# Kernel tuning notes

Measured on AMD Instinct MI355X. Metric: run time of the kernel, lower is better.

Reference implementation:

```python
import jax, jax.numpy as jnp
import numpy as np

N = 40000      # nodes
E = 20000      # hyperedges
M = 640000     # incidences
D = 128        # num_features == num_classes == MLP_hidden
ALPHA = 0.1
EPS = 1e-5


def _layernorm(h, g, b):
    mu = jnp.mean(h, axis=-1, keepdims=True)
    var = jnp.mean((h - mu) ** 2, axis=-1, keepdims=True)
    return (h - mu) * jax.lax.rsqrt(var + EPS) * g + b


def _mlp(x, w1, b1, g, be, w2, b2):
    h = x @ w1 + b1
    h = jax.nn.relu(_layernorm(h, g, be))
    return h @ w2 + b2


def _scatter_mean(vals, idx, num_segments):
    s = jax.ops.segment_sum(vals, idx, num_segments=num_segments)
    cnt = jax.ops.segment_sum(jnp.ones((vals.shape[0],), vals.dtype), idx,
                              num_segments=num_segments)
    return s / jnp.maximum(cnt, 1.0)[:, None]


def setup_inputs() -> dict:
    key = jax.random.key(0)
    ks = jax.random.split(key, 16)
    x = jax.random.normal(ks[0], (N, D), dtype=jnp.float32)
    vertex = jax.random.randint(ks[1], (M,), 0, N)
    edges = jax.random.randint(ks[2], (M,), 0, E)
    edge_index = jnp.stack([vertex, edges]).astype(jnp.int64)

    def lin(k, fin, fout):
        s = 1.0 / np.sqrt(fin)
        kw, kb = jax.random.split(k)
        return (jax.random.uniform(kw, (fin, fout), jnp.float32, -s, s),
                jax.random.uniform(kb, (fout,), jnp.float32, -s, s))

    w1_1, b1_1 = lin(ks[3], D, D)
    w1_2, b1_2 = lin(ks[4], D, D)
    w2_1, b2_1 = lin(ks[5], 2 * D, D)
    w2_2, b2_2 = lin(ks[6], D, D)
    g1 = jnp.ones((D,), jnp.float32)
    be1 = jnp.zeros((D,), jnp.float32)
    g2 = jnp.ones((D,), jnp.float32)
    be2 = jnp.zeros((D,), jnp.float32)
    return {"x": x, "w1_1": w1_1, "b1_1": b1_1, "g1": g1, "be1": be1,
            "w1_2": w1_2, "b1_2": b1_2, "w2_1": w2_1, "b2_1": b2_1,
            "g2": g2, "be2": be2, "w2_2": w2_2, "b2_2": b2_2,
            "edge_index": edge_index}


def reference(x, w1_1, b1_1, g1, be1, w1_2, b1_2,
              w2_1, b2_1, g2, be2, w2_2, b2_2, edge_index):
    vertex = edge_index[0]
    edges = edge_index[1]
    X0 = x
    # gather -> MLP1 -> scatter-mean onto hyperedges
    Xve = _mlp(x[vertex], w1_1, b1_1, g1, be1, w1_2, b1_2)   # [M, D]
    Xe = _scatter_mean(Xve, edges, E)                         # [E, D]
    # gather back -> concat -> MLP2 -> scatter-mean onto nodes
    Xev = Xe[edges]                                           # [M, D]
    Xev = _mlp(jnp.concatenate([x[vertex], Xev], axis=-1),
               w2_1, b2_1, g2, be2, w2_2, b2_2)               # [M, D]
    Xv = _scatter_mean(Xev, vertex, N)                        # [N, D]
    return (1.0 - ALPHA) * Xv + ALPHA * X0
```

## Files before the change

### kernel.cpp

```cpp
#include <hip/hip_runtime.h>

#define DF 128
constexpr int NN = 40000;
constexpr int EE = 20000;
constexpr int MM = 640000;
constexpr float EPSF = 1e-5f;
constexpr float ALPHA = 0.1f;
constexpr int SE = 96;
constexpr int SV = 64;

constexpr int NB_G1 = (NN + 63) / 64;
constexpr int NB_G2 = (NN + 63) / 64;
constexpr int NB_CB = (128 * 128 + 128 + 255) / 256;
constexpr int NB_GEMMS = NB_G1 + NB_G2 + NB_CB;
constexpr int NB_BUILD = 5000;

__device__ __forceinline__ int cidxE(int e) { return (e & 7) * (EE >> 3) + (e >> 3); }
__device__ __forceinline__ int cidxV(int v) { return (v & 7) * (NN >> 3) + (v >> 3); }

template <int EPI, bool STATS>
__device__ __forceinline__ void gemm_tile(const float* __restrict__ A, int nrows,
                                          const float* __restrict__ W,
                                          const float* __restrict__ bias,
                                          const float* __restrict__ bias2,
                                          const int* __restrict__ cnt,
                                          const float* __restrict__ g,
                                          const float* __restrict__ be,
                                          const float* __restrict__ xres,
                                          float* __restrict__ C,
                                          float* __restrict__ sOut,
                                          float* __restrict__ qOut,
                                          int blk, float* as) {
  int tid = threadIdx.x;
  int rbase = blk * 64;

  #pragma unroll
  for (int j = 0; j < 8; ++j) {
    int q = tid + j * 256;
    int row = q >> 5;
    int c4 = q & 31;
    int grow = rbase + row;
    float4 v = make_float4(0.f, 0.f, 0.f, 0.f);
    if (grow < nrows) {
      v = *reinterpret_cast<const float4*>(A + (size_t)grow * DF + c4 * 4);
    }
    *reinterpret_cast<float4*>(&as[row * 132 + c4 * 4]) = v;
  }
  __syncthreads();

  int tc = tid & 15;
  int tr = tid >> 4;
  int cbase = tc * 8;

  float acc[4][8];
  #pragma unroll
  for (int i = 0; i < 4; ++i)
    #pragma unroll
    for (int c = 0; c < 8; ++c) acc[i][c] = 0.0f;

  #pragma unroll 4
  for (int k = 0; k < 128; ++k) {
    float w[8];
    *reinterpret_cast<float4*>(&w[0]) = *reinterpret_cast<const float4*>(W + k * DF + cbase);
    *reinterpret_cast<float4*>(&w[4]) = *reinterpret_cast<const float4*>(W + k * DF + cbase + 4);
    float a[4];
    #pragma unroll
    for (int i = 0; i < 4; ++i) a[i] = as[(tr * 4 + i) * 132 + k];
    #pragma unroll
    for (int i = 0; i < 4; ++i)
      #pragma unroll
      for (int c = 0; c < 8; ++c) acc[i][c] += a[i] * w[c];
  }

  float bv[8];
  #pragma unroll
  for (int c = 0; c < 8; ++c) bv[c] = 0.0f;
  if (bias) {
    #pragma unroll
    for (int c = 0; c < 8; ++c) bv[c] = bias[cbase + c];
  }
  if (bias2) {
    #pragma unroll
    for (int c = 0; c < 8; ++c) bv[c] += bias2[cbase + c];
  }
  #pragma unroll
  for (int i = 0; i < 4; ++i)
    #pragma unroll
    for (int c = 0; c < 8; ++c) acc[i][c] += bv[c];

  if (STATS) {
    #pragma unroll
    for (int i = 0; i < 4; ++i) {
      float s = 0.f, q = 0.f;
      #pragma unroll
      for (int c = 0; c < 8; ++c) { s += acc[i][c]; q += acc[i][c] * acc[i][c]; }
      #pragma unroll
      for (int mask = 1; mask <= 8; mask <<= 1) {
        s += __shfl_xor(s, mask, 16);
        q += __shfl_xor(q, mask, 16);
      }
      if (tc == 0) {
        int grow = rbase + tr * 4 + i;
        if (grow < nrows) { sOut[grow] = s; qOut[grow] = q; }
      }
    }
  }

  if (EPI == 1) {
    float gv[8], bev[8];
    #pragma unroll
    for (int c = 0; c < 8; ++c) { gv[c] = g[cbase + c]; bev[c] = be[cbase + c]; }
    #pragma unroll
    for (int i = 0; i < 4; ++i) {
      float s = 0.f, s2 = 0.f;
      #pragma unroll
      for (int c = 0; c < 8; ++c) { s += acc[i][c]; s2 += acc[i][c] * acc[i][c]; }
      #pragma unroll
      for (int mask = 1; mask <= 8; mask <<= 1) {
        s += __shfl_xor(s, mask, 16);
        s2 += __shfl_xor(s2, mask, 16);
      }
      float mean = s * (1.0f / 128.0f);
      float var = s2 * (1.0f / 128.0f) - mean * mean;
      float rs = rsqrtf(var + EPSF);
      #pragma unroll
      for (int c = 0; c < 8; ++c) {
        float y = (acc[i][c] - mean) * rs * gv[c] + bev[c];
        acc[i][c] = fmaxf(y, 0.0f);
      }
    }
  }

  #pragma unroll
  for (int i = 0; i < 4; ++i) {
    int grow = rbase + tr * 4 + i;
    if (grow >= nrows) continue;
    float outv[8];
    if (EPI == 2) {
      int cv = cnt[(grow & 7) * (NN >> 3) + (grow >> 3)];
      #pragma unroll
      for (int c = 0; c < 8; ++c) {
        float xv = xres[(size_t)grow * DF + cbase + c];
        outv[c] = (cv == 0) ? ALPHA * xv : (1.0f - ALPHA) * acc[i][c] + ALPHA * xv;
      }
    } else {
      #pragma unroll
      for (int c = 0; c < 8; ++c) outv[c] = acc[i][c];
    }
    *reinterpret_cast<float4*>(C + (size_t)grow * DF + cbase) =
        make_float4(outv[0], outv[1], outv[2], outv[3]);
    *reinterpret_cast<float4*>(C + (size_t)grow * DF + cbase + 4) =
        make_float4(outv[4], outv[5], outv[6], outv[7]);
  }
}

__global__ __launch_bounds__(256) void fusedA(
    const int* __restrict__ ei,
    int* __restrict__ cnt_e, int* __restrict__ cnt_v,
    ushort* __restrict__ lst_e, ushort* __restrict__ lst_v,
    const float* __restrict__ x,
    const float* __restrict__ w1_1, const float* __restrict__ b1_1,
    const float* __restrict__ g1, const float* __restrict__ be1,
    const float* __restrict__ w2_1,
    const float* __restrict__ w1_2, const float* __restrict__ b1_2,
    float* __restrict__ H1, float* __restrict__ A2,
    float* __restrict__ sA, float* __restrict__ qA,
    float* __restrict__ Wc, float* __restrict__ bc) {
  __shared__ float as[64 * 132];
  int blk = blockIdx.x;
  if (blk < NB_G1) {
    gemm_tile<1, false>(x, NN, w1_1, b1_1, nullptr, nullptr, g1, be1, nullptr,
                        H1, nullptr, nullptr, blk, as);
  } else if (blk < NB_G1 + NB_G2) {
    gemm_tile<0, true>(x, NN, w2_1, nullptr, nullptr, nullptr, nullptr, nullptr,
                       nullptr, A2, sA, qA, blk - NB_G1, as);
  } else if (blk < NB_GEMMS) {
    const float* w2b = w2_1 + 128 * DF;
    int out = (blk - NB_G1 - NB_G2) * 256 + threadIdx.x;
    if (out < 16384) {
      int i = out >> 7;
      int j = out & 127;
      float s = 0.0f;
      for (int k = 0; k < 128; ++k) s += w1_2[i * DF + k] * w2b[k * DF + j];
      Wc[out] = s;
    } else if (out < 16512) {
      int j = out - 16384;
      float s = 0.0f;
      for (int k = 0; k < 128; ++k) s += b1_2[k] * w2b[k * DF + j];
      bc[j] = s;
    }
  } else {
    int b = blk - NB_GEMMS;
    int role = blk & 7;
    int group = b >> 3;
    #pragma unroll
    for (int k = 0; k < 4; ++k) {
      int m = (group * 4 + k) * 256 + threadIdx.x;
      int v = ei[m];
      int e = ei[MM + m];
      if ((e & 7) == role) {
        int pe = atomicAdd(&cnt_e[role * (EE >> 3) + (e >> 3)], 1);
        lst_e[e * SE + pe] = (ushort)v;
      }
      if ((v & 7) == role) {
        int pv = atomicAdd(&cnt_v[role * (NN >> 3) + (v >> 3)], 1);
        lst_v[v * SV + pv] = (ushort)e;
      }
    }
  }
}

template <int EPI, bool STATS>
__global__ __launch_bounds__(256) void gemm128(const float* __restrict__ A, int nrows,
                                               const float* __restrict__ W,
                                               const float* __restrict__ bias,
                                               const float* __restrict__ bias2,
                                               const int* __restrict__ cnt,
                                               const float* __restrict__ g,
                                               const float* __restrict__ be,
                                               const float* __restrict__ xres,
                                               float* __restrict__ C,
                                               float* __restrict__ sOut,
                                               float* __restrict__ qOut) {
  __shared__ float as[64 * 132];
  gemm_tile<EPI, STATS>(A, nrows, W, bias, bias2, cnt, g, be, xres, C, sOut,
                        qOut, blockIdx.x, as);
}

__global__ __launch_bounds__(256) void gather1(const float* __restrict__ H1,
                                               const int* __restrict__ cnt_e,
                                               const ushort* __restrict__ lst_e,
                                               float* __restrict__ Hemean) {
  int e = blockIdx.x * 4 + (threadIdx.x >> 6);
  int lane = threadIdx.x & 63;
  int g = lane >> 4;
  int l = lane & 15;
  int deg = cnt_e[cidxE(e)];
  const ushort* lst = lst_e + e * SE;
  float4 acc0 = make_float4(0.f, 0.f, 0.f, 0.f);
  float4 acc1 = make_float4(0.f, 0.f, 0.f, 0.f);
  for (int i = g; i < deg; i += 4) {
    int v = lst[i];
    const float* src = H1 + (size_t)v * DF + l * 8;
    float4 h0 = *reinterpret_cast<const float4*>(src);
    float4 h1 = *reinterpret_cast<const float4*>(src + 4);
    acc0.x += h0.x; acc0.y += h0.y; acc0.z += h0.z; acc0.w += h0.w;
    acc1.x += h1.x; acc1.y += h1.y; acc1.z += h1.z; acc1.w += h1.w;
  }
  #pragma unroll
  for (int mask = 16; mask <= 32; mask <<= 1) {
    acc0.x += __shfl_xor(acc0.x, mask); acc0.y += __shfl_xor(acc0.y, mask);
    acc0.z += __shfl_xor(acc0.z, mask); acc0.w += __shfl_xor(acc0.w, mask);
    acc1.x += __shfl_xor(acc1.x, mask); acc1.y += __shfl_xor(acc1.y, mask);
    acc1.z += __shfl_xor(acc1.z, mask); acc1.w += __shfl_xor(acc1.w, mask);
  }
  if (g == 0) {
    float sc = 1.0f / (float)(deg > 1 ? deg : 1);
    float* dst = Hemean + (size_t)e * DF + l * 8;
    *reinterpret_cast<float4*>(dst) =
        make_float4(acc0.x * sc, acc0.y * sc, acc0.z * sc, acc0.w * sc);
    *reinterpret_cast<float4*>(dst + 4) =
        make_float4(acc1.x * sc, acc1.y * sc, acc1.z * sc, acc1.w * sc);
  }
}

__global__ __launch_bounds__(256) void gather2(const float* __restrict__ A2,
                                               const float* __restrict__ B,
                                               const float* __restrict__ sA,
                                               const float* __restrict__ qA,
                                               const float* __restrict__ sB,
                                               const float* __restrict__ qB,
                                               const int* __restrict__ cnt_v,
                                               const ushort* __restrict__ lst_v,
                                               const float* __restrict__ g2,
                                               const float* __restrict__ be2,
                                               float* __restrict__ Svmean) {
  int v = blockIdx.x * 4 + (threadIdx.x >> 6);
  int lane = threadIdx.x & 63;
  int g = lane >> 4;
  int l = lane & 15;
  const float* ap = A2 + (size_t)v * DF + l * 8;
  float4 a0 = *reinterpret_cast<const float4*>(ap);
  float4 a1 = *reinterpret_cast<const float4*>(ap + 4);
  float4 gv0 = *reinterpret_cast<const float4*>(g2 + l * 8);
  float4 gv1 = *reinterpret_cast<const float4*>(g2 + l * 8 + 4);
  float4 bv0 = *reinterpret_cast<const float4*>(be2 + l * 8);
  float4 bv1 = *reinterpret_cast<const float4*>(be2 + l * 8 + 4);
  float sAv = sA[v];
  float qAv = qA[v];
  int deg = cnt_v[cidxV(v)];
  const ushort* lst = lst_v + v * SV;
  float4 acc0 = make_float4(0.f, 0.f, 0.f, 0.f);
  float4 acc1 = make_float4(0.f, 0.f, 0.f, 0.f);
  for (int i = g; i < deg; i += 4) {
    int e = lst[i];
    const float* bp = B + (size_t)e * DF + l * 8;
    float4 b0 = *reinterpret_cast<const float4*>(bp);
    float4 b1 = *reinterpret_cast<const float4*>(bp + 4);
    float d = a0.x * b0.x + a0.y * b0.y + a0.z * b0.z + a0.w * b0.w +
              a1.x * b1.x + a1.y * b1.y + a1.z * b1.z + a1.w * b1.w;
    d += __shfl_xor(d, 1, 16);
    d += __shfl_xor(d, 2, 16);
    d += __shfl_xor(d, 4, 16);
    d += __shfl_xor(d, 8, 16);
    float s = sAv + sB[e];
    float q = qAv + qB[e] + 2.0f * d;
    float mean = s * (1.0f / 128.0f);
    float var = q * (1.0f / 128.0f) - mean * mean;
    float rs = rsqrtf(var + EPSF);
    float mrs = mean * rs;
    float t;
    t = (a0.x + b0.x) * rs - mrs; acc0.x += fmaxf(t * gv0.x + bv0.x, 0.f);
    t = (a0.y + b0.y) * rs - mrs; acc0.y += fmaxf(t * gv0.y + bv0.y, 0.f);
    t = (a0.z + b0.z) * rs - mrs; acc0.z += fmaxf(t * gv0.z + bv0.z, 0.f);
    t = (a0.w + b0.w) * rs - mrs; acc0.w += fmaxf(t * gv0.w + bv0.w, 0.f);
    t = (a1.x + b1.x) * rs - mrs; acc1.x += fmaxf(t * gv1.x + bv1.x, 0.f);
    t = (a1.y + b1.y) * rs - mrs; acc1.y += fmaxf(t * gv1.y + bv1.y, 0.f);
    t = (a1.z + b1.z) * rs - mrs; acc1.z += fmaxf(t * gv1.z + bv1.z, 0.f);
    t = (a1.w + b1.w) * rs - mrs; acc1.w += fmaxf(t * gv1.w + bv1.w, 0.f);
  }
  #pragma unroll
  for (int mask = 16; mask <= 32; mask <<= 1) {
    acc0.x += __shfl_xor(acc0.x, mask); acc0.y += __shfl_xor(acc0.y, mask);
    acc0.z += __shfl_xor(acc0.z, mask); acc0.w += __shfl_xor(acc0.w, mask);
    acc1.x += __shfl_xor(acc1.x, mask); acc1.y += __shfl_xor(acc1.y, mask);
    acc1.z += __shfl_xor(acc1.z, mask); acc1.w += __shfl_xor(acc1.w, mask);
  }
  if (g == 0) {
    float sc = 1.0f / (float)(deg > 1 ? deg : 1);
    float* dst = Svmean + (size_t)v * DF + l * 8;
    *reinterpret_cast<float4*>(dst) =
        make_float4(acc0.x * sc, acc0.y * sc, acc0.z * sc, acc0.w * sc);
    *reinterpret_cast<float4*>(dst + 4) =
        make_float4(acc1.x * sc, acc1.y * sc, acc1.z * sc, acc1.w * sc);
  }
}

extern "C" void kernel_launch(void* const* d_in, const int* in_sizes, int n_in,
                              void* d_out, int out_size, void* d_ws, size_t ws_size,
                              hipStream_t stream) {
  const float* x    = (const float*)d_in[0];
  const float* w1_1 = (const float*)d_in[1];
  const float* b1_1 = (const float*)d_in[2];
  const float* g1   = (const float*)d_in[3];
  const float* be1  = (const float*)d_in[4];
  const float* w1_2 = (const float*)d_in[5];
  const float* b1_2 = (const float*)d_in[6];
  const float* w2_1 = (const float*)d_in[7];
  const float* b2_1 = (const float*)d_in[8];
  const float* g2   = (const float*)d_in[9];
  const float* be2  = (const float*)d_in[10];
  const float* w2_2 = (const float*)d_in[11];
  const float* b2_2 = (const float*)d_in[12];
  const int* ei     = (const int*)d_in[13];
  float* out = (float*)d_out;

  float* ws = (float*)d_ws;
  float* bufN1 = ws;
  float* bufN2 = ws + 5120000;
  float* bufE  = ws + 10240000;
  float* Wc    = ws + 12800000;
  float* bc    = ws + 12816384;
  float* sA    = ws + 12816512;
  float* qA    = ws + 12856512;
  float* sB    = ws + 12896512;
  float* qB    = ws + 12916512;
  int*   ints  = (int*)(ws + 12936512);
  int* cnt_e  = ints;
  int* cnt_v  = ints + 20000;
  ushort* lst_e = (ushort*)(ints + 60000);
  ushort* lst_v = (ushort*)(ints + 60000 + 960000);

  hipMemsetAsync(cnt_e, 0, 60000 * sizeof(int), stream);

  fusedA<<<NB_GEMMS + NB_BUILD, 256, 0, stream>>>(
      ei, cnt_e, cnt_v, lst_e, lst_v, x, w1_1, b1_1, g1, be1, w2_1, w1_2, b1_2,
      bufN1, bufN2, sA, qA, Wc, bc);

  gather1<<<EE / 4, 256, 0, stream>>>(bufN1, cnt_e, lst_e, bufE);

  gemm128<0, true><<<(EE + 63) / 64, 256, 0, stream>>>(
      bufE, EE, Wc, bc, b2_1, nullptr, nullptr, nullptr, nullptr, bufE, sB, qB);

  gather2<<<NN / 4, 256, 0, stream>>>(bufN2, bufE, sA, qA, sB, qB,
                                      cnt_v, lst_v, g2, be2, bufN1);

  gemm128<2, false><<<(NN + 63) / 64, 256, 0, stream>>>(
      bufN1, NN, w2_2, b2_2, nullptr, cnt_v, nullptr, nullptr, x, out,
      nullptr, nullptr);
}
```

Baseline: 331.4 us.

## Apply folded edge-side linear map per node before hyperedge mean

```diff
diff --git a/kernel.cpp b/kernel.cpp
--- a/kernel.cpp
+++ b/kernel.cpp
@@ -11,172 +11,25 @@
 
 constexpr int NB_G1 = (NN + 63) / 64;
 constexpr int NB_G2 = (NN + 63) / 64;
-constexpr int NB_CB = (128 * 128 + 128 + 255) / 256;
-constexpr int NB_GEMMS = NB_G1 + NB_G2 + NB_CB;
+constexpr int NB_GEMMS = NB_G1 + NB_G2;
 constexpr int NB_BUILD = 5000;
 
 __device__ __forceinline__ int cidxE(int e) { return (e & 7) * (EE >> 3) + (e >> 3); }
 __device__ __forceinline__ int cidxV(int v) { return (v & 7) * (NN >> 3) + (v >> 3); }
 
-template <int EPI, bool STATS>
-__device__ __forceinline__ void gemm_tile(const float* __restrict__ A, int nrows,
-                                          const float* __restrict__ W,
-                                          const float* __restrict__ bias,
-                                          const float* __restrict__ bias2,
-                                          const int* __restrict__ cnt,
-                                          const float* __restrict__ g,
-                                          const float* __restrict__ be,
-                                          const float* __restrict__ xres,
-                                          float* __restrict__ C,
-                                          float* __restrict__ sOut,
-                                          float* __restrict__ qOut,
-                                          int blk, float* as) {
-  int tid = threadIdx.x;
-  int rbase = blk * 64;
-
-  #pragma unroll
-  for (int j = 0; j < 8; ++j) {
-    int q = tid + j * 256;
-    int row = q >> 5;
-    int c4 = q & 31;
-    int grow = rbase + row;
-    float4 v = make_float4(0.f, 0.f, 0.f, 0.f);
-    if (grow < nrows) {
-      v = *reinterpret_cast<const float4*>(A + (size_t)grow * DF + c4 * 4);
-    }
-    *reinterpret_cast<float4*>(&as[row * 132 + c4 * 4]) = v;
-  }
-  __syncthreads();
-
-  int tc = tid & 15;
-  int tr = tid >> 4;
-  int cbase = tc * 8;
-
-  float acc[4][8];
-  #pragma unroll
-  for (int i = 0; i < 4; ++i)
-    #pragma unroll
-    for (int c = 0; c < 8; ++c) acc[i][c] = 0.0f;
-
-  #pragma unroll 4
-  for (int k = 0; k < 128; ++k) {
-    float w[8];
-    *reinterpret_cast<float4*>(&w[0]) = *reinterpret_cast<const float4*>(W + k * DF + cbase);
-    *reinterpret_cast<float4*>(&w[4]) = *reinterpret_cast<const float4*>(W + k * DF + cbase + 4);
-    float a[4];
-    #pragma unroll
-    for (int i = 0; i < 4; ++i) a[i] = as[(tr * 4 + i) * 132 + k];
-    #pragma unroll
-    for (int i = 0; i < 4; ++i)
-      #pragma unroll
-      for (int c = 0; c < 8; ++c) acc[i][c] += a[i] * w[c];
-  }
-
-  float bv[8];
-  #pragma unroll
-  for (int c = 0; c < 8; ++c) bv[c] = 0.0f;
-  if (bias) {
-    #pragma unroll
-    for (int c = 0; c < 8; ++c) bv[c] = bias[cbase + c];
-  }
-  if (bias2) {
-    #pragma unroll
-    for (int c = 0; c < 8; ++c) bv[c] += bias2[cbase + c];
-  }
-  #pragma unroll
-  for (int i = 0; i < 4; ++i)
-    #pragma unroll
-    for (int c = 0; c < 8; ++c) acc[i][c] += bv[c];
-
-  if (STATS) {
-    #pragma unroll
-    for (int i = 0; i < 4; ++i) {
-      float s = 0.f, q = 0.f;
-      #pragma unroll
-      for (int c = 0; c < 8; ++c) { s += acc[i][c]; q += acc[i][c] * acc[i][c]; }
-      #pragma unroll
-      for (int mask = 1; mask <= 8; mask <<= 1) {
-        s += __shfl_xor(s, mask, 16);
-        q += __shfl_xor(q, mask, 16);
-      }
-      if (tc == 0) {
-        int grow = rbase + tr * 4 + i;
-        if (grow < nrows) { sOut[grow] = s; qOut[grow] = q; }
-      }
-    }
-  }
-
-  if (EPI == 1) {
-    float gv[8], bev[8];
-    #pragma unroll
-    for (int c = 0; c < 8; ++c) { gv[c] = g[cbase + c]; bev[c] = be[cbase + c]; }
-    #pragma unroll
-    for (int i = 0; i < 4; ++i) {
-      float s = 0.f, s2 = 0.f;
-      #pragma unroll
-      for (int c = 0; c < 8; ++c) { s += acc[i][c]; s2 += acc[i][c] * acc[i][c]; }
-      #pragma unroll
-      for (int mask = 1; mask <= 8; mask <<= 1) {
-        s += __shfl_xor(s, mask, 16);
-        s2 += __shfl_xor(s2, mask, 16);
-      }
-      float mean = s * (1.0f / 128.0f);
-      float var = s2 * (1.0f / 128.0f) - mean * mean;
-      float rs = rsqrtf(var + EPSF);
-      #pragma unroll
-      for (int c = 0; c < 8; ++c) {
-        float y = (acc[i][c] - mean) * rs * gv[c] + bev[c];
-        acc[i][c] = fmaxf(y, 0.0f);
-      }
-    }
-  }
-
-  #pragma unroll
-  for (int i = 0; i < 4; ++i) {
-    int grow = rbase + tr * 4 + i;
-    if (grow >= nrows) continue;
-    float outv[8];
-    if (EPI == 2) {
-      int cv = cnt[(grow & 7) * (NN >> 3) + (grow >> 3)];
-      #pragma unroll
-      for (int c = 0; c < 8; ++c) {
-        float xv = xres[(size_t)grow * DF + cbase + c];
-        outv[c] = (cv == 0) ? ALPHA * xv : (1.0f - ALPHA) * acc[i][c] + ALPHA * xv;
-      }
-    } else {
-      #pragma unroll
-      for (int c = 0; c < 8; ++c) outv[c] = acc[i][c];
-    }
-    *reinterpret_cast<float4*>(C + (size_t)grow * DF + cbase) =
-        make_float4(outv[0], outv[1], outv[2], outv[3]);
-    *reinterpret_cast<float4*>(C + (size_t)grow * DF + cbase + 4) =
-        make_float4(outv[4], outv[5], outv[6], outv[7]);
-  }
-}
-
-__global__ __launch_bounds__(256) void fusedA(
-    const int* __restrict__ ei,
-    int* __restrict__ cnt_e, int* __restrict__ cnt_v,
-    ushort* __restrict__ lst_e, ushort* __restrict__ lst_v,
-    const float* __restrict__ x,
-    const float* __restrict__ w1_1, const float* __restrict__ b1_1,
-    const float* __restrict__ g1, const float* __restrict__ be1,
-    const float* __restrict__ w2_1,
-    const float* __restrict__ w1_2, const float* __restrict__ b1_2,
-    float* __restrict__ H1, float* __restrict__ A2,
-    float* __restrict__ sA, float* __restrict__ qA,
-    float* __restrict__ Wc, float* __restrict__ bc) {
-  __shared__ float as[64 * 132];
-  int blk = blockIdx.x;
-  if (blk < NB_G1) {
-    gemm_tile<1, false>(x, NN, w1_1, b1_1, nullptr, nullptr, g1, be1, nullptr,
-                        H1, nullptr, nullptr, blk, as);
-  } else if (blk < NB_G1 + NB_G2) {
-    gemm_tile<0, true>(x, NN, w2_1, nullptr, nullptr, nullptr, nullptr, nullptr,
-                       nullptr, A2, sA, qA, blk - NB_G1, as);
-  } else if (blk < NB_GEMMS) {
+__global__ __launch_bounds__(256) void prek(int* __restrict__ cnt,
+                                            const float* __restrict__ w1_2,
+                                            const float* __restrict__ b1_2,
+                                            const float* __restrict__ w2_1,
+                                            float* __restrict__ Wc,
+                                            float* __restrict__ bc) {
+  int b = blockIdx.x;
+  if (b < 235) {
+    int i = b * 256 + threadIdx.x;
+    if (i < 60000) cnt[i] = 0;
+  } else {
     const float* w2b = w2_1 + 128 * DF;
-    int out = (blk - NB_G1 - NB_G2) * 256 + threadIdx.x;
+    int out = (b - 235) * 256 + threadIdx.x;
     if (out < 16384) {
       int i = out >> 7;
       int j = out & 127;
@@ -189,6 +42,236 @@
       for (int k = 0; k < 128; ++k) s += b1_2[k] * w2b[k * DF + j];
       bc[j] = s;
     }
+  }
+}
+
+template <int EPI, bool STATS>
+__device__ __forceinline__ void gemm_tile(const float* __restrict__ A, int nrows,
+                                          const float* __restrict__ W,
+                                          const float* __restrict__ bias,
+                                          const int* __restrict__ cnt,
+                                          const float* __restrict__ xres,
+                                          float* __restrict__ C,
+                                          float* __restrict__ sOut,
+                                          float* __restrict__ qOut,
+                                          int blk, float* as) {
+  int tid = threadIdx.x;
+  int rbase = blk * 64;
+
+  #pragma unroll
+  for (int j = 0; j < 8; ++j) {
+    int q = tid + j * 256;
+    int row = q >> 5;
+    int c4 = q & 31;
+    int grow = rbase + row;
+    float4 v = make_float4(0.f, 0.f, 0.f, 0.f);
+    if (grow < nrows) {
+      v = *reinterpret_cast<const float4*>(A + (size_t)grow * DF + c4 * 4);
+    }
+    *reinterpret_cast<float4*>(&as[row * 132 + c4 * 4]) = v;
+  }
+  __syncthreads();
+
+  int tc = tid & 15;
+  int tr = tid >> 4;
+  int cbase = tc * 8;
+
+  float acc[4][8];
+  #pragma unroll
+  for (int i = 0; i < 4; ++i)
+    #pragma unroll
+    for (int c = 0; c < 8; ++c) acc[i][c] = 0.0f;
+
+  #pragma unroll 4
+  for (int k = 0; k < 128; ++k) {
+    float w[8];
+    *reinterpret_cast<float4*>(&w[0]) = *reinterpret_cast<const float4*>(W + k * DF + cbase);
+    *reinterpret_cast<float4*>(&w[4]) = *reinterpret_cast<const float4*>(W + k * DF + cbase + 4);
+    float a[4];
+    #pragma unroll
+    for (int i = 0; i < 4; ++i) a[i] = as[(tr * 4 + i) * 132 + k];
+    #pragma unroll
+    for (int i = 0; i < 4; ++i)
+      #pragma unroll
+      for (int c = 0; c < 8; ++c) acc[i][c] += a[i] * w[c];
+  }
+
+  if (bias) {
+    #pragma unroll
+    for (int i = 0; i < 4; ++i)
+      #pragma unroll
+      for (int c = 0; c < 8; ++c) acc[i][c] += bias[cbase + c];
+  }
+
+  if (STATS) {
+    #pragma unroll
+    for (int i = 0; i < 4; ++i) {
+      float s = 0.f, q = 0.f;
+      #pragma unroll
+      for (int c = 0; c < 8; ++c) { s += acc[i][c]; q += acc[i][c] * acc[i][c]; }
+      #pragma unroll
+      for (int mask = 1; mask <= 8; mask <<= 1) {
+        s += __shfl_xor(s, mask, 16);
+        q += __shfl_xor(q, mask, 16);
+      }
+      if (tc == 0) {
+        int grow = rbase + tr * 4 + i;
+        if (grow < nrows) { sOut[grow] = s; qOut[grow] = q; }
+      }
+    }
+  }
+
+  #pragma unroll
+  for (int i = 0; i < 4; ++i) {
+    int grow = rbase + tr * 4 + i;
+    if (grow >= nrows) continue;
+    float outv[8];
+    if (EPI == 2) {
+      int cv = cnt[(grow & 7) * (NN >> 3) + (grow >> 3)];
+      #pragma unroll
+      for (int c = 0; c < 8; ++c) {
+        float xv = xres[(size_t)grow * DF + cbase + c];
+        outv[c] = (cv == 0) ? ALPHA * xv : (1.0f - ALPHA) * acc[i][c] + ALPHA * xv;
+      }
+    } else {
+      #pragma unroll
+      for (int c = 0; c < 8; ++c) outv[c] = acc[i][c];
+    }
+    *reinterpret_cast<float4*>(C + (size_t)grow * DF + cbase) =
+        make_float4(outv[0], outv[1], outv[2], outv[3]);
+    *reinterpret_cast<float4*>(C + (size_t)grow * DF + cbase + 4) =
+        make_float4(outv[4], outv[5], outv[6], outv[7]);
+  }
+}
+
+__device__ __forceinline__ void gemm_tile_double(const float* __restrict__ x,
+                                                 const float* __restrict__ W1,
+                                                 const float* __restrict__ b1,
+                                                 const float* __restrict__ g,
+                                                 const float* __restrict__ be,
+                                                 const float* __restrict__ W2,
+                                                 float* __restrict__ G,
+                                                 int blk, float* as) {
+  int tid = threadIdx.x;
+  int rbase = blk * 64;
+
+  #pragma unroll
+  for (int j = 0; j < 8; ++j) {
+    int q = tid + j * 256;
+    int row = q >> 5;
+    int c4 = q & 31;
+    int grow = rbase + row;
+    float4 v = make_float4(0.f, 0.f, 0.f, 0.f);
+    if (grow < NN) {
+      v = *reinterpret_cast<const float4*>(x + (size_t)grow * DF + c4 * 4);
+    }
+    *reinterpret_cast<float4*>(&as[row * 132 + c4 * 4]) = v;
+  }
+  __syncthreads();
+
+  int tc = tid & 15;
+  int tr = tid >> 4;
+  int cbase = tc * 8;
+
+  float acc[4][8];
+  #pragma unroll
+  for (int i = 0; i < 4; ++i)
+    #pragma unroll
+    for (int c = 0; c < 8; ++c) acc[i][c] = 0.0f;
+
+  #pragma unroll 4
+  for (int k = 0; k < 128; ++k) {
+    float w[8];
+    *reinterpret_cast<float4*>(&w[0]) = *reinterpret_cast<const float4*>(W1 + k * DF + cbase);
+    *reinterpret_cast<float4*>(&w[4]) = *reinterpret_cast<const float4*>(W1 + k * DF + cbase + 4);
+    float a[4];
+    #pragma unroll
+    for (int i = 0; i < 4; ++i) a[i] = as[(tr * 4 + i) * 132 + k];
+    #pragma unroll
+    for (int i = 0; i < 4; ++i)
+      #pragma unroll
+      for (int c = 0; c < 8; ++c) acc[i][c] += a[i] * w[c];
+  }
+
+  float gv[8], bev[8];
+  #pragma unroll
+  for (int c = 0; c < 8; ++c) { gv[c] = g[cbase + c]; bev[c] = be[cbase + c]; }
+  #pragma unroll
+  for (int i = 0; i < 4; ++i) {
+    #pragma unroll
+    for (int c = 0; c < 8; ++c) acc[i][c] += b1[cbase + c];
+    float s = 0.f, s2 = 0.f;
+    #pragma unroll
+    for (int c = 0; c < 8; ++c) { s += acc[i][c]; s2 += acc[i][c] * acc[i][c]; }
+    #pragma unroll
+    for (int mask = 1; mask <= 8; mask <<= 1) {
+      s += __shfl_xor(s, mask, 16);
+      s2 += __shfl_xor(s2, mask, 16);
+    }
+    float mean = s * (1.0f / 128.0f);
+    float var = s2 * (1.0f / 128.0f) - mean * mean;
+    float rs = rsqrtf(var + EPSF);
+    #pragma unroll
+    for (int c = 0; c < 8; ++c) {
+      float y = (acc[i][c] - mean) * rs * gv[c] + bev[c];
+      acc[i][c] = fmaxf(y, 0.0f);
+    }
+  }
+
+  __syncthreads();
+  #pragma unroll
+  for (int i = 0; i < 4; ++i)
+    #pragma unroll
+    for (int c = 0; c < 8; ++c) as[(tr * 4 + i) * 132 + cbase + c] = acc[i][c];
+  __syncthreads();
+
+  #pragma unroll
+  for (int i = 0; i < 4; ++i)
+    #pragma unroll
+    for (int c = 0; c < 8; ++c) acc[i][c] = 0.0f;
+
+  #pragma unroll 4
+  for (int k = 0; k < 128; ++k) {
+    float w[8];
+    *reinterpret_cast<float4*>(&w[0]) = *reinterpret_cast<const float4*>(W2 + k * DF + cbase);
+    *reinterpret_cast<float4*>(&w[4]) = *reinterpret_cast<const float4*>(W2 + k * DF + cbase + 4);
+    float a[4];
+    #pragma unroll
+    for (int i = 0; i < 4; ++i) a[i] = as[(tr * 4 + i) * 132 + k];
+    #pragma unroll
+    for (int i = 0; i < 4; ++i)
+      #pragma unroll
+      for (int c = 0; c < 8; ++c) acc[i][c] += a[i] * w[c];
+  }
+
+  #pragma unroll
+  for (int i = 0; i < 4; ++i) {
+    int grow = rbase + tr * 4 + i;
+    if (grow >= NN) continue;
+    *reinterpret_cast<float4*>(G + (size_t)grow * DF + cbase) =
+        make_float4(acc[i][0], acc[i][1], acc[i][2], acc[i][3]);
+    *reinterpret_cast<float4*>(G + (size_t)grow * DF + cbase + 4) =
+        make_float4(acc[i][4], acc[i][5], acc[i][6], acc[i][7]);
+  }
+}
+
+__global__ __launch_bounds__(256) void fusedA(
+    const int* __restrict__ ei,
+    int* __restrict__ cnt_e, int* __restrict__ cnt_v,
+    ushort* __restrict__ lst_e, ushort* __restrict__ lst_v,
+    const float* __restrict__ x,
+    const float* __restrict__ w1_1, const float* __restrict__ b1_1,
+    const float* __restrict__ g1, const float* __restrict__ be1,
+    const float* __restrict__ w2_1, const float* __restrict__ Wc,
+    float* __restrict__ G, float* __restrict__ A2,
+    float* __restrict__ sA, float* __restrict__ qA) {
+  __shared__ float as[64 * 132];
+  int blk = blockIdx.x;
+  if (blk < NB_G1) {
+    gemm_tile_double(x, w1_1, b1_1, g1, be1, Wc, G, blk, as);
+  } else if (blk < NB_GEMMS) {
+    gemm_tile<0, true>(x, NN, w2_1, nullptr, nullptr, nullptr, A2, sA, qA,
+                       blk - NB_G1, as);
   } else {
     int b = blk - NB_GEMMS;
     int role = blk & 7;
@@ -214,23 +297,24 @@
 __global__ __launch_bounds__(256) void gemm128(const float* __restrict__ A, int nrows,
                                                const float* __restrict__ W,
                                                const float* __restrict__ bias,
-                                               const float* __restrict__ bias2,
                                                const int* __restrict__ cnt,
-                                               const float* __restrict__ g,
-                                               const float* __restrict__ be,
                                                const float* __restrict__ xres,
                                                float* __restrict__ C,
                                                float* __restrict__ sOut,
                                                float* __restrict__ qOut) {
   __shared__ float as[64 * 132];
-  gemm_tile<EPI, STATS>(A, nrows, W, bias, bias2, cnt, g, be, xres, C, sOut,
-                        qOut, blockIdx.x, as);
-}
-
-__global__ __launch_bounds__(256) void gather1(const float* __restrict__ H1,
-                                               const int* __restrict__ cnt_e,
-                                               const ushort* __restrict__ lst_e,
-                                               float* __restrict__ Hemean) {
+  gemm_tile<EPI, STATS>(A, nrows, W, bias, cnt, xres, C, sOut, qOut,
+                        blockIdx.x, as);
+}
+
+__global__ __launch_bounds__(256) void gather1B(const float* __restrict__ G,
+                                                const int* __restrict__ cnt_e,
+                                                const ushort* __restrict__ lst_e,
+                                                const float* __restrict__ bcv,
+                                                const float* __restrict__ b21,
+                                                float* __restrict__ B,
+                                                float* __restrict__ sB,
+                                                float* __restrict__ qB) {
   int e = blockIdx.x * 4 + (threadIdx.x >> 6);
   int lane = threadIdx.x & 63;
   int g = lane >> 4;
@@ -241,7 +325,7 @@
   float4 acc1 = make_float4(0.f, 0.f, 0.f, 0.f);
   for (int i = g; i < deg; i += 4) {
     int v = lst[i];
-    const float* src = H1 + (size_t)v * DF + l * 8;
+    const float* src = G + (size_t)v * DF + l * 8;
     float4 h0 = *reinterpret_cast<const float4*>(src);
     float4 h1 = *reinterpret_cast<const float4*>(src + 4);
     acc0.x += h0.x; acc0.y += h0.y; acc0.z += h0.z; acc0.w += h0.w;
@@ -256,11 +340,27 @@
   }
   if (g == 0) {
     float sc = 1.0f / (float)(deg > 1 ? deg : 1);
-    float* dst = Hemean + (size_t)e * DF + l * 8;
-    *reinterpret_cast<float4*>(dst) =
-        make_float4(acc0.x * sc, acc0.y * sc, acc0.z * sc, acc0.w * sc);
-    *reinterpret_cast<float4*>(dst + 4) =
-        make_float4(acc1.x * sc, acc1.y * sc, acc1.z * sc, acc1.w * sc);
+    float b[8];
+    b[0] = acc0.x * sc + bcv[l * 8 + 0] + b21[l * 8 + 0];
+    b[1] = acc0.y * sc + bcv[l * 8 + 1] + b21[l * 8 + 1];
+    b[2] = acc0.z * sc + bcv[l * 8 + 2] + b21[l * 8 + 2];
+    b[3] = acc0.w * sc + bcv[l * 8 + 3] + b21[l * 8 + 3];
+    b[4] = acc1.x * sc + bcv[l * 8 + 4] + b21[l * 8 + 4];
+    b[5] = acc1.y * sc + bcv[l * 8 + 5] + b21[l * 8 + 5];
+    b[6] = acc1.z * sc + bcv[l * 8 + 6] + b21[l * 8 + 6];
+    b[7] = acc1.w * sc + bcv[l * 8 + 7] + b21[l * 8 + 7];
+    float* dst = B + (size_t)e * DF + l * 8;
+    *reinterpret_cast<float4*>(dst) = make_float4(b[0], b[1], b[2], b[3]);
+    *reinterpret_cast<float4*>(dst + 4) = make_float4(b[4], b[5], b[6], b[7]);
+    float s = 0.f, q = 0.f;
+    #pragma unroll
+    for (int j = 0; j < 8; ++j) { s += b[j]; q += b[j] * b[j]; }
+    #pragma unroll
+    for (int mask = 1; mask <= 8; mask <<= 1) {
+      s += __shfl_xor(s, mask, 16);
+      q += __shfl_xor(q, mask, 16);
+    }
+    if (l == 0) { sB[e] = s; qB[e] = q; }
   }
 }
 
@@ -371,21 +471,18 @@
   ushort* lst_e = (ushort*)(ints + 60000);
   ushort* lst_v = (ushort*)(ints + 60000 + 960000);
 
-  hipMemsetAsync(cnt_e, 0, 60000 * sizeof(int), stream);
+  prek<<<300, 256, 0, stream>>>(cnt_e, w1_2, b1_2, w2_1, Wc, bc);
 
   fusedA<<<NB_GEMMS + NB_BUILD, 256, 0, stream>>>(
-      ei, cnt_e, cnt_v, lst_e, lst_v, x, w1_1, b1_1, g1, be1, w2_1, w1_2, b1_2,
-      bufN1, bufN2, sA, qA, Wc, bc);
-
-  gather1<<<EE / 4, 256, 0, stream>>>(bufN1, cnt_e, lst_e, bufE);
-
-  gemm128<0, true><<<(EE + 63) / 64, 256, 0, stream>>>(
-      bufE, EE, Wc, bc, b2_1, nullptr, nullptr, nullptr, nullptr, bufE, sB, qB);
+      ei, cnt_e, cnt_v, lst_e, lst_v, x, w1_1, b1_1, g1, be1, w2_1, Wc,
+      bufN1, bufN2, sA, qA);
+
+  gather1B<<<EE / 4, 256, 0, stream>>>(bufN1, cnt_e, lst_e, bc, b2_1,
+                                       bufE, sB, qB);
 
   gather2<<<NN / 4, 256, 0, stream>>>(bufN2, bufE, sA, qA, sB, qB,
                                       cnt_v, lst_v, g2, be2, bufN1);
 
   gemm128<2, false><<<(NN + 63) / 64, 256, 0, stream>>>(
-      bufN1, NN, w2_2, b2_2, nullptr, cnt_v, nullptr, nullptr, x, out,
-      nullptr, nullptr);
-}
+      bufN1, NN, w2_2, b2_2, cnt_v, x, out, nullptr, nullptr);
+}
```

Result: no change. 327.1 us (-1.3%).
